# Kernel optimization log

Measured on AMD Instinct MI355X. Metric: run time of the kernel, lower is better.

The kernel has to match this reference:

```python
import jax, jax.numpy as jnp
import numpy as np

B, LQ, LK, E, H = 8, 1024, 1024, 512, 8
D = E // H
NEG = -2.0**32 + 1  # padding value used by original torch code


def setup_inputs() -> dict:
    key = jax.random.key(0)
    ks = jax.random.split(key, 6)
    s = 0.02
    return {
        "x1": jax.random.normal(ks[0], (B, LQ, E), jnp.float32),
        "x2": jax.random.normal(ks[1], (B, LK, E), jnp.float32),
        "Wq": jax.random.normal(ks[2], (E, E), jnp.float32) * s,
        "bq": jnp.zeros((E,), jnp.float32),
        "Wk": jax.random.normal(ks[3], (E, E), jnp.float32) * s,
        "bk": jnp.zeros((E,), jnp.float32),
        "Wv": jax.random.normal(ks[4], (E, E), jnp.float32) * s,
        "bv": jnp.zeros((E,), jnp.float32),
    }


def _split_heads(t):
    # torch: cat(split(t, E//H, dim=2), dim=0) -> head-major [H, B, L, D]
    b, l, _ = t.shape
    return jnp.moveaxis(t.reshape(b, l, H, D), 2, 0)


def reference(x1, x2, Wq, bq, Wk, bk, Wv, bv):
    # ReLU-activated projections (nn.Linear: x @ W.T + b)
    q = jax.nn.relu(x1 @ Wq.T + bq)  # [B,LQ,E]
    k = jax.nn.relu(x2 @ Wk.T + bk)  # [B,LK,E]
    v = jax.nn.relu(x2 @ Wv.T + bv)  # [B,LK,E]

    q_, k_, v_ = _split_heads(q), _split_heads(k), _split_heads(v)  # [H,B,L,D]

    # scaled scores; original scales by sqrt(emb_size), not sqrt(d_head)
    scores = jnp.einsum('hbqd,hbkd->hbqk', q_, k_) / jnp.sqrt(jnp.float32(E))

    # sin-based key mask from raw x2
    key_mask = jnp.sin(jnp.abs(jnp.sum(x2, -1)))  # [B,LK]
    scores = jnp.where(key_mask[None, :, None, :] <= 0, NEG, scores)

    attn = jax.nn.softmax(scores, axis=-1)

    # sin-based query mask from raw x1, applied after softmax
    query_mask = jnp.sin(jnp.abs(jnp.sum(x1, -1)))  # [B,LQ]
    attn = attn * query_mask[None, :, :, None]

    out = jnp.einsum('hbqk,hbkd->hbqd', attn, v_)  # [H,B,LQ,D]
    out = jnp.moveaxis(out, 0, 2).reshape(B, LQ, E)  # merge heads back
    return out + q  # residual add with activated query projection
```

## Files before the change

### kernel.cpp

```cpp
#include <hip/hip_runtime.h>
#include <hip/hip_bf16.h>
#include <math.h>

typedef short bf16x8 __attribute__((ext_vector_type(8)));
typedef float f32x4 __attribute__((ext_vector_type(4)));
typedef unsigned int u32;
typedef unsigned short u16;

constexpr int Bb = 8, LQn = 1024, LKn = 1024, En = 512, Hn = 8, Dn = 64;
constexpr int Mtok = Bb * LQn;
constexpr float KCOEF = 0.06376246332977306f;

__device__ __forceinline__ u16 f2bf(float f) {
  u32 u = __builtin_bit_cast(u32, f);
  u32 r = (u + 0x7fffu + ((u >> 16) & 1u)) >> 16;
  return (u16)r;
}
__device__ __forceinline__ float bf2f(u16 h) {
  u32 u = ((u32)h) << 16;
  return __builtin_bit_cast(float, u);
}
__device__ __forceinline__ u16 f2bf_hw(float f) {
  return __builtin_bit_cast(u16, __float2bfloat16(f));
}

__device__ __forceinline__ void async_lds16(const void* gsrc, void* ldst) {
  __builtin_amdgcn_global_load_lds(
      (const __attribute__((address_space(1))) u32*)gsrc,
      (__attribute__((address_space(3))) u32*)ldst, 16, 0, 0);
}

__global__ void prep_kernel(const float* __restrict__ x1, const float* __restrict__ x2,
                            u16* __restrict__ x1b, u16* __restrict__ x2b,
                            float* __restrict__ qmask, float* __restrict__ kbias,
                            const float* __restrict__ Wq, const float* __restrict__ Wk,
                            const float* __restrict__ Wv, u16* __restrict__ wqb,
                            u16* __restrict__ wkb, u16* __restrict__ wvb) {
  int blk = blockIdx.x;
  if (blk < 4096) {
    int id = blk * 4 + (threadIdx.x >> 6);
    int lane = threadIdx.x & 63;
    const float* x; u16* xb; int row; bool isq;
    if (id < Mtok) { x = x1; xb = x1b; row = id; isq = true; }
    else           { x = x2; xb = x2b; row = id - Mtok; isq = false; }
    const float4* p = reinterpret_cast<const float4*>(x + (size_t)row * En);
    ushort4* ob = reinterpret_cast<ushort4*>(xb + (size_t)row * En);
    double s = 0.0;
#pragma unroll
    for (int j = 0; j < En / 256; ++j) {
      float4 v = p[lane + j * 64];
      s += (double)v.x + (double)v.y + (double)v.z + (double)v.w;
      ushort4 o;
      o.x = f2bf(v.x); o.y = f2bf(v.y); o.z = f2bf(v.z); o.w = f2bf(v.w);
      ob[lane + j * 64] = o;
    }
#pragma unroll
    for (int off = 32; off > 0; off >>= 1) s += __shfl_down(s, off, 64);
    if (lane == 0) {
      float sv = (float)sin(fabs(s));
      if (isq) qmask[row] = sv;
      else     kbias[row] = sv > 0.f ? 0.f : -3.0e38f;
    }
  } else {
    int n4 = En * En / 4;
    int j = (blk - 4096) * 256 + threadIdx.x;
    const float* src; u16* dst;
    if (j < n4) { src = Wq; dst = wqb; }
    else if (j < 2 * n4) { src = Wk; dst = wkb; j -= n4; }
    else { src = Wv; dst = wvb; j -= 2 * n4; }
    float4 v = reinterpret_cast<const float4*>(src)[j];
    ushort4 o;
    o.x = f2bf(v.x); o.y = f2bf(v.y); o.z = f2bf(v.z); o.w = f2bf(v.w);
    reinterpret_cast<ushort4*>(dst)[j] = o;
  }
}

template <int BIAS_ROW>
__device__ __forceinline__ void gemm_core(
    const u16* __restrict__ A, const u16* __restrict__ Bm,
    const float* __restrict__ bias, u16* __restrict__ C,
    int ldc, float coef, int row0, int col0) {
  constexpr int K = 512, BK = 64;
  __shared__ u16 sA[128 * BK];
  __shared__ u16 sB[128 * BK];
  int tid = threadIdx.x;
  int lane = tid & 63;
  int w = tid >> 6;
  int wm = w >> 2, wn = w & 3;
  int rgrp = lane >> 4, cidx = lane & 15;

  f32x4 acc[4][2];
#pragma unroll
  for (int mi = 0; mi < 4; ++mi)
#pragma unroll
    for (int ni = 0; ni < 2; ++ni) acc[mi][ni] = f32x4{0.f, 0.f, 0.f, 0.f};

  for (int kt = 0; kt < K / BK; ++kt) {
    int k0 = kt * BK;
    __syncthreads();
#pragma unroll
    for (int rr = 0; rr < 2; ++rr) {
      int cid = rr * 512 + tid;
      int r = cid >> 3, c = cid & 7;
      int cg = c ^ (r & 7);
      async_lds16(A + (size_t)(row0 + r) * K + k0 + cg * 8, &sA[cid * 8]);
    }
#pragma unroll
    for (int rr = 0; rr < 2; ++rr) {
      int cid = rr * 512 + tid;
      int r = cid >> 3, c = cid & 7;
      int cg = c ^ (r & 7);
      async_lds16(Bm + (size_t)(col0 + r) * K + k0 + cg * 8, &sB[cid * 8]);
    }
    __syncthreads();
#pragma unroll
    for (int kk = 0; kk < 2; ++kk) {
      bf16x8 a[4], b[2];
#pragma unroll
      for (int mi = 0; mi < 4; ++mi) {
        int row = wm * 64 + mi * 16 + cidx;
        a[mi] = *reinterpret_cast<const bf16x8*>(
            &sA[row * BK + ((kk * 4 + rgrp) ^ (row & 7)) * 8]);
      }
#pragma unroll
      for (int ni = 0; ni < 2; ++ni) {
        int row = wn * 32 + ni * 16 + cidx;
        b[ni] = *reinterpret_cast<const bf16x8*>(
            &sB[row * BK + ((kk * 4 + rgrp) ^ (row & 7)) * 8]);
      }
#pragma unroll
      for (int mi = 0; mi < 4; ++mi)
#pragma unroll
        for (int ni = 0; ni < 2; ++ni)
          acc[mi][ni] = __builtin_amdgcn_mfma_f32_16x16x32_bf16(a[mi], b[ni], acc[mi][ni], 0, 0, 0);
    }
  }
#pragma unroll
  for (int mi = 0; mi < 4; ++mi)
#pragma unroll
    for (int ni = 0; ni < 2; ++ni)
#pragma unroll
      for (int r = 0; r < 4; ++r) {
        int grow = row0 + wm * 64 + mi * 16 + rgrp * 4 + r;
        int gcol = col0 + wn * 32 + ni * 16 + cidx;
        float v = acc[mi][ni][r] + (BIAS_ROW ? bias[grow] : bias[gcol]);
        v = v > 0.f ? v : 0.f;
        C[(size_t)grow * ldc + gcol] = f2bf_hw(v * coef);
      }
}

__global__ __launch_bounds__(512, 6) void gemm3(
    const u16* __restrict__ x1b, const u16* __restrict__ wqb, const float* __restrict__ bq,
    u16* __restrict__ qbq,
    const u16* __restrict__ x2b, const u16* __restrict__ wkb, const float* __restrict__ bk,
    u16* __restrict__ kbk,
    const u16* __restrict__ wvb, const float* __restrict__ bv, u16* __restrict__ vtb) {
  int z = blockIdx.z;
  if (z == 0) {
    gemm_core<0>(x1b, wqb, bq, qbq, En, 1.0f, blockIdx.x * 128, blockIdx.y * 128);
  } else if (z == 1) {
    gemm_core<0>(x2b, wkb, bk, kbk, En, KCOEF, blockIdx.x * 128, blockIdx.y * 128);
  } else {
    gemm_core<1>(wvb, x2b, bv, vtb, Mtok, 1.0f, blockIdx.y * 128, blockIdx.x * 128);
  }
}

__global__ __launch_bounds__(256, 4) void attn_kernel(
    const u16* __restrict__ qb, const u16* __restrict__ kb, const u16* __restrict__ vtb,
    const float* __restrict__ kbias, const float* __restrict__ qmask,
    float* __restrict__ out) {
  __shared__ u16 sK[2][64 * 64];
  __shared__ u16 sV[2][64 * 64];
  __shared__ u16 sQP[64 * 64];
  int tid = threadIdx.x, lane = tid & 63, w = tid >> 6;
  int bh = blockIdx.x, qblk = blockIdx.y;
  int b = bh >> 3, h = bh & 7;
  int rgrp = lane >> 4, cidx = lane & 15;

  const u16* qbase = qb + ((size_t)(b * LQn) + qblk * 64) * En + h * Dn;
  const u16* kbase = kb + (size_t)(b * LKn) * En + h * Dn;
  const u16* vbase = vtb + (size_t)(h * Dn) * Mtok + b * LKn;
  const float* kmb = kbias + b * LKn;

  int scid0 = tid, scid1 = 256 + tid;
  int sr0 = scid0 >> 3, sc0 = (scid0 & 7) ^ (sr0 & 7);
  int sr1 = scid1 >> 3, sc1 = (scid1 & 7) ^ (sr1 & 7);
  auto stageKV = [&](int kt, int buf) {
    async_lds16(kbase + (size_t)(kt * 64 + sr0) * En + sc0 * 8, &sK[buf][scid0 * 8]);
    async_lds16(vbase + (size_t)sr0 * Mtok + kt * 64 + sc0 * 8, &sV[buf][scid0 * 8]);
    async_lds16(kbase + (size_t)(kt * 64 + sr1) * En + sc1 * 8, &sK[buf][scid1 * 8]);
    async_lds16(vbase + (size_t)sr1 * Mtok + kt * 64 + sc1 * 8, &sV[buf][scid1 * 8]);
  };

#pragma unroll
  for (int rr = 0; rr < 2; ++rr) {
    int cid = rr * 256 + tid;
    int r = cid >> 3, c = cid & 7;
    int cg = c ^ (r & 7);
    async_lds16(qbase + (size_t)r * En + cg * 8, &sQP[cid * 8]);
  }
  stageKV(0, 0);
  __syncthreads();

  bf16x8 qa0, qa1;
  {
    int row = w * 16 + cidx;
    qa0 = *reinterpret_cast<const bf16x8*>(&sQP[row * 64 + (rgrp ^ (row & 7)) * 8]);
    qa1 = *reinterpret_cast<const bf16x8*>(&sQP[row * 64 + ((4 + rgrp) ^ (row & 7)) * 8]);
  }
  bf16x8 ones;
#pragma unroll
  for (int e = 0; e < 8; ++e) ones[e] = (short)0x3F80;

  char* sKb = reinterpret_cast<char*>(sK);
  char* sVb = reinterpret_cast<char*>(sV);
  char* sPbyte = reinterpret_cast<char*>(sQP);
  int prow = w * 16 + cidx;
  u32 koffb[4][2];
#pragma unroll
  for (int ktile = 0; ktile < 4; ++ktile) {
    int krow = ktile * 16 + cidx;
    koffb[ktile][0] = (u32)(krow * 128 + ((rgrp ^ (krow & 7)) * 16));
    koffb[ktile][1] = (u32)(krow * 128 + (((4 + rgrp) ^ (krow & 7)) * 16));
  }
  u32 voffb[2][4];
#pragma unroll
  for (int kk = 0; kk < 2; ++kk)
#pragma unroll
    for (int dt = 0; dt < 4; ++dt) {
      int vrow = dt * 16 + cidx;
      voffb[kk][dt] = (u32)(vrow * 128 + (((kk * 4 + rgrp) ^ (vrow & 7)) * 16));
    }
  u32 pwoff[4];
#pragma unroll
  for (int ktile = 0; ktile < 4; ++ktile) {
    int gran = ktile * 2 + (rgrp >> 1);
    pwoff[ktile] = (u32)(prow * 128 + ((gran ^ (prow & 7)) << 4) + ((rgrp & 1) << 3));
  }
  u32 paoff[2];
#pragma unroll
  for (int kk = 0; kk < 2; ++kk)
    paoff[kk] = (u32)(prow * 128 + (((kk * 4 + rgrp) ^ (prow & 7)) * 16));

  f32x4 acc_o[4];
#pragma unroll
  for (int dt = 0; dt < 4; ++dt) acc_o[dt] = f32x4{0.f, 0.f, 0.f, 0.f};
  f32x4 acc_den = f32x4{0.f, 0.f, 0.f, 0.f};

  const float* kmrow = kmb + rgrp * 4;

  for (int kt2 = 0; kt2 < 8; ++kt2) {
#pragma unroll
    for (int half = 0; half < 2; ++half) {
      int kt = kt2 * 2 + half;
      if (kt < 15) stageKV(kt + 1, half ^ 1);
#pragma unroll
      for (int ktile = 0; ktile < 4; ++ktile) {
        bf16x8 kf0 = *reinterpret_cast<const bf16x8*>(sKb + half * 8192 + koffb[ktile][0]);
        bf16x8 kf1 = *reinterpret_cast<const bf16x8*>(sKb + half * 8192 + koffb[ktile][1]);
        float4 km4 = *reinterpret_cast<const float4*>(kmrow + ktile * 16);
        f32x4 s;
        s[0] = km4.x; s[1] = km4.y; s[2] = km4.z; s[3] = km4.w;
        s = __builtin_amdgcn_mfma_f32_16x16x32_bf16(kf0, qa0, s, 0, 0, 0);
        s = __builtin_amdgcn_mfma_f32_16x16x32_bf16(kf1, qa1, s, 0, 0, 0);
        float p0 = __builtin_amdgcn_exp2f(s[0]);
        float p1 = __builtin_amdgcn_exp2f(s[1]);
        float p2 = __builtin_amdgcn_exp2f(s[2]);
        float p3 = __builtin_amdgcn_exp2f(s[3]);
        u32 w0, w1;
        asm("v_cvt_pk_bf16_f32 %0, %1, %2" : "=v"(w0) : "v"(p0), "v"(p1));
        asm("v_cvt_pk_bf16_f32 %0, %1, %2" : "=v"(w1) : "v"(p2), "v"(p3));
        uint2 pk2; pk2.x = w0; pk2.y = w1;
        *reinterpret_cast<uint2*>(sPbyte + pwoff[ktile]) = pk2;
      }
      __builtin_amdgcn_s_setprio(1);
#pragma unroll
      for (int kk = 0; kk < 2; ++kk) {
        bf16x8 pa = *reinterpret_cast<const bf16x8*>(sPbyte + paoff[kk]);
        acc_den = __builtin_amdgcn_mfma_f32_16x16x32_bf16(pa, ones, acc_den, 0, 0, 0);
#pragma unroll
        for (int dt = 0; dt < 4; ++dt) {
          bf16x8 vf = *reinterpret_cast<const bf16x8*>(sVb + half * 8192 + voffb[kk][dt]);
          acc_o[dt] = __builtin_amdgcn_mfma_f32_16x16x32_bf16(pa, vf, acc_o[dt], 0, 0, 0);
        }
      }
      __builtin_amdgcn_s_setprio(0);
      kmrow += 64;
      __syncthreads();
    }
  }

  const float* qmb = qmask + (size_t)b * LQn + qblk * 64 + w * 16;
  const u16* qres = qbase + (size_t)(w * 16) * En;
  float* obase = out + ((size_t)(b * LQn) + qblk * 64 + w * 16) * En + h * Dn;
#pragma unroll
  for (int r = 0; r < 4; ++r) {
    int qr = rgrp * 4 + r;
    float fac = qmb[qr] / acc_den[r];
#pragma unroll
    for (int dt = 0; dt < 4; ++dt) {
      float v = acc_o[dt][r] * fac + bf2f(qres[(size_t)qr * En + dt * 16 + cidx]);
      obase[(size_t)qr * En + dt * 16 + cidx] = v;
    }
  }
}

extern "C" void kernel_launch(void* const* d_in, const int* in_sizes, int n_in,
                              void* d_out, int out_size, void* d_ws, size_t ws_size,
                              hipStream_t stream) {
  const float* x1 = (const float*)d_in[0];
  const float* x2 = (const float*)d_in[1];
  const float* Wq = (const float*)d_in[2];
  const float* bq = (const float*)d_in[3];
  const float* Wk = (const float*)d_in[4];
  const float* bk = (const float*)d_in[5];
  const float* Wv = (const float*)d_in[6];
  const float* bv = (const float*)d_in[7];
  float* out = (float*)d_out;

  char* ws = (char*)d_ws;
  size_t o = 0;
  u16* x1b = (u16*)(ws + o); o += (size_t)Mtok * En * 2;
  u16* x2b = (u16*)(ws + o); o += (size_t)Mtok * En * 2;
  u16* wqb = (u16*)(ws + o); o += (size_t)En * En * 2;
  u16* wkb = (u16*)(ws + o); o += (size_t)En * En * 2;
  u16* wvb = (u16*)(ws + o); o += (size_t)En * En * 2;
  u16* qbq = (u16*)(ws + o); o += (size_t)Mtok * En * 2;
  u16* kbk = (u16*)(ws + o); o += (size_t)Mtok * En * 2;
  u16* vtb = (u16*)(ws + o); o += (size_t)Mtok * En * 2;
  float* kbias = (float*)(ws + o); o += (size_t)Mtok * 4;
  float* qmask = (float*)(ws + o); o += (size_t)Mtok * 4;

  prep_kernel<<<4864, 256, 0, stream>>>(x1, x2, x1b, x2b, qmask, kbias,
                                        Wq, Wk, Wv, wqb, wkb, wvb);

  dim3 g3(Mtok / 128, En / 128, 3);
  gemm3<<<g3, 512, 0, stream>>>(x1b, wqb, bq, qbq, x2b, wkb, bk, kbk, wvb, bv, vtb);

  dim3 ga(Bb * Hn, LQn / 64);
  attn_kernel<<<ga, 256, 0, stream>>>(qbq, kbk, vtb, kbias, qmask, out);
}
```

Baseline: 64.49 us.

## Split K/V async waits with partial vmcnt and peel last iterations

Reorders the async K/V prefetch so both K loads are issued before the V loads. It then replaces the full __syncthreads with explicit partial vmcnt waits plus raw s_barrier: the QK phase waits only for the K tile and the PV phase waits for V. The last two iterations are peeled so the final wait drains to zero. The aim is to keep V loads in flight while QK runs, letting the async prefetch overlap compute instead of stalling on a full drain. The cost is reliance on exact async-load counting and ordering for correctness.

```diff
diff --git a/kernel.cpp b/kernel.cpp
--- a/kernel.cpp
+++ b/kernel.cpp
@@ -187,8 +187,8 @@
   int sr1 = scid1 >> 3, sc1 = (scid1 & 7) ^ (sr1 & 7);
   auto stageKV = [&](int kt, int buf) {
     async_lds16(kbase + (size_t)(kt * 64 + sr0) * En + sc0 * 8, &sK[buf][scid0 * 8]);
+    async_lds16(kbase + (size_t)(kt * 64 + sr1) * En + sc1 * 8, &sK[buf][scid1 * 8]);
     async_lds16(vbase + (size_t)sr0 * Mtok + kt * 64 + sc0 * 8, &sV[buf][scid0 * 8]);
-    async_lds16(kbase + (size_t)(kt * 64 + sr1) * En + sc1 * 8, &sK[buf][scid1 * 8]);
     async_lds16(vbase + (size_t)sr1 * Mtok + kt * 64 + sc1 * 8, &sV[buf][scid1 * 8]);
   };
 
@@ -249,46 +249,78 @@
 
   const float* kmrow = kmb + rgrp * 4;
 
-  for (int kt2 = 0; kt2 < 8; ++kt2) {
+#define ATTN_QK(half)                                                              \
+  _Pragma("unroll")                                                                \
+  for (int ktile = 0; ktile < 4; ++ktile) {                                        \
+    bf16x8 kf0 = *reinterpret_cast<const bf16x8*>(sKb + (half)*8192 + koffb[ktile][0]); \
+    bf16x8 kf1 = *reinterpret_cast<const bf16x8*>(sKb + (half)*8192 + koffb[ktile][1]); \
+    float4 km4 = *reinterpret_cast<const float4*>(kmrow + ktile * 16);             \
+    f32x4 s;                                                                       \
+    s[0] = km4.x; s[1] = km4.y; s[2] = km4.z; s[3] = km4.w;                        \
+    s = __builtin_amdgcn_mfma_f32_16x16x32_bf16(kf0, qa0, s, 0, 0, 0);             \
+    s = __builtin_amdgcn_mfma_f32_16x16x32_bf16(kf1, qa1, s, 0, 0, 0);             \
+    float p0 = __builtin_amdgcn_exp2f(s[0]);                                       \
+    float p1 = __builtin_amdgcn_exp2f(s[1]);                                       \
+    float p2 = __builtin_amdgcn_exp2f(s[2]);                                       \
+    float p3 = __builtin_amdgcn_exp2f(s[3]);                                       \
+    u32 w0, w1;                                                                    \
+    asm("v_cvt_pk_bf16_f32 %0, %1, %2" : "=v"(w0) : "v"(p0), "v"(p1));             \
+    asm("v_cvt_pk_bf16_f32 %0, %1, %2" : "=v"(w1) : "v"(p2), "v"(p3));             \
+    uint2 pk2; pk2.x = w0; pk2.y = w1;                                             \
+    *reinterpret_cast<uint2*>(sPbyte + pwoff[ktile]) = pk2;                        \
+  }
+
+#define ATTN_PV(half)                                                              \
+  __builtin_amdgcn_s_setprio(1);                                                   \
+  _Pragma("unroll")                                                                \
+  for (int kk = 0; kk < 2; ++kk) {                                                 \
+    bf16x8 pa = *reinterpret_cast<const bf16x8*>(sPbyte + paoff[kk]);              \
+    acc_den = __builtin_amdgcn_mfma_f32_16x16x32_bf16(pa, ones, acc_den, 0, 0, 0); \
+    _Pragma("unroll")                                                              \
+    for (int dt = 0; dt < 4; ++dt) {                                               \
+      bf16x8 vf = *reinterpret_cast<const bf16x8*>(sVb + (half)*8192 + voffb[kk][dt]); \
+      acc_o[dt] = __builtin_amdgcn_mfma_f32_16x16x32_bf16(pa, vf, acc_o[dt], 0, 0, 0); \
+    }                                                                              \
+  }                                                                                \
+  __builtin_amdgcn_s_setprio(0);
+
+  for (int kt2 = 0; kt2 < 7; ++kt2) {
 #pragma unroll
     for (int half = 0; half < 2; ++half) {
       int kt = kt2 * 2 + half;
-      if (kt < 15) stageKV(kt + 1, half ^ 1);
-#pragma unroll
-      for (int ktile = 0; ktile < 4; ++ktile) {
-        bf16x8 kf0 = *reinterpret_cast<const bf16x8*>(sKb + half * 8192 + koffb[ktile][0]);
-        bf16x8 kf1 = *reinterpret_cast<const bf16x8*>(sKb + half * 8192 + koffb[ktile][1]);
-        float4 km4 = *reinterpret_cast<const float4*>(kmrow + ktile * 16);
-        f32x4 s;
-        s[0] = km4.x; s[1] = km4.y; s[2] = km4.z; s[3] = km4.w;
-        s = __builtin_amdgcn_mfma_f32_16x16x32_bf16(kf0, qa0, s, 0, 0, 0);
-        s = __builtin_amdgcn_mfma_f32_16x16x32_bf16(kf1, qa1, s, 0, 0, 0);
-        float p0 = __builtin_amdgcn_exp2f(s[0]);
-        float p1 = __builtin_amdgcn_exp2f(s[1]);
-        float p2 = __builtin_amdgcn_exp2f(s[2]);
-        float p3 = __builtin_amdgcn_exp2f(s[3]);
-        u32 w0, w1;
-        asm("v_cvt_pk_bf16_f32 %0, %1, %2" : "=v"(w0) : "v"(p0), "v"(p1));
-        asm("v_cvt_pk_bf16_f32 %0, %1, %2" : "=v"(w1) : "v"(p2), "v"(p3));
-        uint2 pk2; pk2.x = w0; pk2.y = w1;
-        *reinterpret_cast<uint2*>(sPbyte + pwoff[ktile]) = pk2;
-      }
-      __builtin_amdgcn_s_setprio(1);
-#pragma unroll
-      for (int kk = 0; kk < 2; ++kk) {
-        bf16x8 pa = *reinterpret_cast<const bf16x8*>(sPbyte + paoff[kk]);
-        acc_den = __builtin_amdgcn_mfma_f32_16x16x32_bf16(pa, ones, acc_den, 0, 0, 0);
-#pragma unroll
-        for (int dt = 0; dt < 4; ++dt) {
-          bf16x8 vf = *reinterpret_cast<const bf16x8*>(sVb + half * 8192 + voffb[kk][dt]);
-          acc_o[dt] = __builtin_amdgcn_mfma_f32_16x16x32_bf16(pa, vf, acc_o[dt], 0, 0, 0);
-        }
-      }
-      __builtin_amdgcn_s_setprio(0);
+      stageKV(kt + 1, half ^ 1);
+      ATTN_QK(half)
+      asm volatile("s_waitcnt vmcnt(4)" ::: "memory");
+      __builtin_amdgcn_sched_barrier(0);
+      __builtin_amdgcn_s_barrier();
+      ATTN_PV(half)
+      asm volatile("s_waitcnt vmcnt(2)" ::: "memory");
+      __builtin_amdgcn_sched_barrier(0);
+      __builtin_amdgcn_s_barrier();
       kmrow += 64;
-      __syncthreads();
-    }
-  }
+    }
+  }
+  {
+    stageKV(15, 1);
+    ATTN_QK(0)
+    asm volatile("s_waitcnt vmcnt(4)" ::: "memory");
+    __builtin_amdgcn_sched_barrier(0);
+    __builtin_amdgcn_s_barrier();
+    ATTN_PV(0)
+    asm volatile("s_waitcnt vmcnt(2)" ::: "memory");
+    __builtin_amdgcn_sched_barrier(0);
+    __builtin_amdgcn_s_barrier();
+    kmrow += 64;
+  }
+  {
+    ATTN_QK(1)
+    asm volatile("s_waitcnt vmcnt(0)" ::: "memory");
+    __builtin_amdgcn_sched_barrier(0);
+    __builtin_amdgcn_s_barrier();
+    ATTN_PV(1)
+  }
+#undef ATTN_QK
+#undef ATTN_PV
 
   const float* qmb = qmask + (size_t)b * LQn + qblk * 64 + w * 16;
   const u16* qres = qbase + (size_t)(w * 16) * En;
```

After: 65.11 us. About the same (+1.0%).
